# Performance work log

Hardware: AMD Instinct MI355X
Metric: run time of the kernel (lower is better)

## Reference

```python
import jax, jax.numpy as jnp
import numpy as np

N, E = 30000, 480000
D_IN, D_HID = 128, 256
NODE_CLS, EDGE_CLS, POLAR = 5, 2, 6
EPS = 1e-5

def layer_norm(x, g, b):
    mu = jnp.mean(x, axis=-1, keepdims=True)
    var = jnp.mean((x - mu) ** 2, axis=-1, keepdims=True)
    return g * (x - mu) / jnp.sqrt(var + EPS) + b

def sage_pool(h, src, dst, Wp, bp, Ws, bs, Wn, n_nodes):
    # DGL SAGEConv aggregator_type='pool': m = relu(fc_pool(h_src)); max over in-edges
    m = jax.nn.relu(h @ Wp + bp)              # [N, d_in]
    agg = jax.ops.segment_max(m[src], dst, num_segments=n_nodes)  # [N, d_in], -inf if no in-edges
    deg = jax.ops.segment_sum(jnp.ones((src.shape[0],), jnp.float32), dst, num_segments=n_nodes)
    h_neigh = jnp.where(deg[:, None] > 0, agg, 0.0)
    out = h @ Ws + bs + h_neigh @ Wn          # fc_self + fc_neigh
    return jax.nn.relu(out)                   # activation=F.relu

def setup_inputs() -> dict:
    key = jax.random.key(0)
    ks = jax.random.split(key, 24)
    p = lambda k, shape, fan: jax.random.normal(k, shape, jnp.float32) / np.sqrt(fan)
    return {
        "h": jax.random.normal(ks[0], (N, D_IN), jnp.float32),
        "efeat": jax.random.normal(ks[1], (E, POLAR), jnp.float32),
        "src": jax.random.randint(ks[2], (E,), 0, N, jnp.int32),
        "dst": jax.random.randint(ks[3], (E,), 0, N, jnp.int32),
        # encoder SAGEConv(128->256)
        "enc_Wpool": p(ks[4], (D_IN, D_IN), D_IN), "enc_bpool": jnp.zeros((D_IN,), jnp.float32),
        "enc_Wself": p(ks[5], (D_IN, D_HID), D_IN), "enc_bself": jnp.zeros((D_HID,), jnp.float32),
        "enc_Wneigh": p(ks[6], (D_IN, D_HID), D_IN),
        # node_pred: Linear(256,5) + LayerNorm(5)
        "np_W": p(ks[7], (D_HID, NODE_CLS), D_HID), "np_b": jnp.zeros((NODE_CLS,), jnp.float32),
        "np_g": jnp.ones((NODE_CLS,), jnp.float32), "np_beta": jnp.zeros((NODE_CLS,), jnp.float32),
        # edge predictor: Linear(528,256) + LN(256) + Linear(256,2)
        "ep_W1": p(ks[8], (2 * D_HID + 2 * NODE_CLS + POLAR, D_HID), 2 * D_HID + 16),
        "ep_b1": jnp.zeros((D_HID,), jnp.float32),
        "ep_g": jnp.ones((D_HID,), jnp.float32), "ep_beta": jnp.zeros((D_HID,), jnp.float32),
        "ep_W2": p(ks[9], (D_HID, EDGE_CLS), D_HID), "ep_b2": jnp.zeros((EDGE_CLS,), jnp.float32),
        # decoder SAGEConv(256->128)
        "dec_Wpool": p(ks[10], (D_HID, D_HID), D_HID), "dec_bpool": jnp.zeros((D_HID,), jnp.float32),
        "dec_Wself": p(ks[11], (D_HID, D_IN), D_HID), "dec_bself": jnp.zeros((D_IN,), jnp.float32),
        "dec_Wneigh": p(ks[12], (D_HID, D_IN), D_HID),
    }

def reference(h, efeat, src, dst,
              enc_Wpool, enc_bpool, enc_Wself, enc_bself, enc_Wneigh,
              np_W, np_b, np_g, np_beta,
              ep_W1, ep_b1, ep_g, ep_beta, ep_W2, ep_b2,
              dec_Wpool, dec_bpool, dec_Wself, dec_bself, dec_Wneigh):
    # encoder (drop_rate == 0 path)
    h1 = sage_pool(h, src, dst, enc_Wpool, enc_bpool, enc_Wself, enc_bself, enc_Wneigh, N)
    # node head
    node_pred = layer_norm(h1 @ np_W + np_b, np_g, np_beta)  # [N, 5]
    # edge head: gather-concat-MLP per edge
    cls_sm = jax.nn.softmax(node_pred, axis=1)               # softmax once, gather per edge
    x = jnp.concatenate([h1[src], cls_sm[src], efeat, h1[dst], cls_sm[dst]], axis=1)  # [E, 528]
    x = jax.nn.relu(layer_norm(x @ ep_W1 + ep_b1, ep_g, ep_beta))
    edges_pred = x @ ep_W2 + ep_b2                           # dropout is identity in eval
    # decoder (uses original graph, input h1)
    h2 = sage_pool(h1, src, dst, dec_Wpool, dec_bpool, dec_Wself, dec_bself, dec_Wneigh, N)
    return (node_pred, edges_pred, h2)
```

## Files before the change

### kernel.cpp

```cpp
#include <hip/hip_runtime.h>

typedef unsigned short u16;
typedef unsigned int u32;
typedef __bf16 bf16_t;
typedef bf16_t bf16x8 __attribute__((ext_vector_type(8)));
typedef float f32x4 __attribute__((ext_vector_type(4)));
typedef float f32x2 __attribute__((ext_vector_type(2)));

#define N_NODES 30000
#define N_EDGES 480000

static __device__ __forceinline__ float b2f(u16 u) {
  return __uint_as_float(((u32)u) << 16);
}
static __device__ __forceinline__ float b2f_lo(u32 w) {
  return __uint_as_float(w << 16);
}
static __device__ __forceinline__ float b2f_hi(u32 w) {
  return __uint_as_float(w & 0xffff0000u);
}
static __device__ __forceinline__ u16 f2b(float f) {
  u32 x = __float_as_uint(f);
  u32 r = (x + 0x7fffu + ((x >> 16) & 1u)) >> 16;
  return (u16)r;
}

__global__ __launch_bounds__(256) void init_sniff_deg(const u16* __restrict__ h,
                                                      int* __restrict__ flag,
                                                      int* __restrict__ deg) {
  int i = blockIdx.x * 256 + threadIdx.x;
  if (i < N_NODES) deg[i] = 0;
  if (blockIdx.x == 0) {
    int t = threadIdx.x;
    int bad = 0;
#pragma unroll
    for (int j = 0; j < 4; j++) {
      u32 e = ((u32)h[t * 4 + j] >> 7) & 0xFFu;
      if (e >= 0x8Eu) bad = 1;
    }
    int r = __syncthreads_or(bad);
    if (t == 0) *flag = r ? 1 : 0;
  }
}

struct ConvDesc { const void* s; u16* d; int n; int off; };
struct ConvTab { ConvDesc e[20]; int total; };

__global__ __launch_bounds__(256) void conv_all(
    const int* __restrict__ dstE, int* __restrict__ deg,
    const void* __restrict__ hsrc, u16* __restrict__ c_h,
    const void* __restrict__ efsrc, u16* __restrict__ c_ef,
    ConvTab tab, const int* __restrict__ flag) {
  int b = blockIdx.x;
  const int t = threadIdx.x;
  if (b < 1875) {
    int e = b * 256 + t;
    if (e < N_EDGES) atomicAdd(&deg[dstE[e]], 1);
    return;
  }
  b -= 1875;
  const int f = *flag;
  if (b < 3750) {
    int i = b * 256 + t;
    if (f) {
      float4 v = ((const float4*)hsrc)[i];
      uint2 o;
      o.x = (u32)f2b(v.x) | ((u32)f2b(v.y) << 16);
      o.y = (u32)f2b(v.z) | ((u32)f2b(v.w) << 16);
      ((uint2*)c_h)[i] = o;
    } else {
      ((uint2*)c_h)[i] = ((const uint2*)hsrc)[i];
    }
    return;
  }
  b -= 3750;
  if (b < 2813) {
    int i = b * 256 + t;
    if (i < 720000) {
      if (f) {
        float4 v = ((const float4*)efsrc)[i];
        uint2 o;
        o.x = (u32)f2b(v.x) | ((u32)f2b(v.y) << 16);
        o.y = (u32)f2b(v.z) | ((u32)f2b(v.w) << 16);
        ((uint2*)c_ef)[i] = o;
      } else {
        ((uint2*)c_ef)[i] = ((const uint2*)efsrc)[i];
      }
    }
    return;
  }
  b -= 2813;
  int i = b * 256 + t;
  if (i >= tab.total) return;
#pragma unroll 1
  for (int a = 0; a < 20; a++) {
    int j = i - tab.e[a].off;
    if (j >= 0 && j < tab.e[a].n) {
      if (f) tab.e[a].d[j] = f2b(((const float*)tab.e[a].s)[j]);
      else tab.e[a].d[j] = ((const u16*)tab.e[a].s)[j];
      return;
    }
  }
}

__global__ __launch_bounds__(1024) void scan_off(const int* __restrict__ deg,
                                                 int* __restrict__ off,
                                                 int* __restrict__ cursor, int n) {
  __shared__ int wsum[16];
  const int t = threadIdx.x, lane = t & 63, wv = t >> 6;
  const int CH = 30;
  int base = t * CH;
  int v[CH];
  int s = 0;
#pragma unroll
  for (int j = 0; j < CH; j++) {
    int idx = base + j;
    int d = (idx < n) ? deg[idx] : 0;
    v[j] = s;
    s += d;
  }
  int x = s;
#pragma unroll
  for (int d = 1; d < 64; d <<= 1) {
    int y = __shfl_up(x, d, 64);
    if (lane >= d) x += y;
  }
  if (lane == 63) wsum[wv] = x;
  __syncthreads();
  int wadd = 0;
  for (int w = 0; w < wv; w++) wadd += wsum[w];
  int pref = (x - s) + wadd;
  if (t == 0) off[0] = 0;
#pragma unroll
  for (int j = 0; j < CH; j++) {
    int idx = base + j;
    if (idx < n) {
      int excl = pref + v[j];
      int incl = pref + ((j + 1 < CH) ? v[j + 1] : s);
      cursor[idx] = excl;
      off[idx + 1] = incl;
    }
  }
}

__global__ __launch_bounds__(256) void fill_csr(const int* __restrict__ src,
                                                const int* __restrict__ dst,
                                                int* __restrict__ cursor,
                                                int* __restrict__ esrc, int nE) {
  int e = blockIdx.x * 256 + threadIdx.x;
  if (e >= nE) return;
  int p = atomicAdd(&cursor[dst[e]], 1);
  esrc[p] = src[e];
}

#define MRG(r)                                                    \
  do {                                                            \
    a0 = max(a0, (r).x & 0xffffu); a1 = max(a1, (r).x >> 16);     \
    a2 = max(a2, (r).y & 0xffffu); a3 = max(a3, (r).y >> 16);     \
    a4 = max(a4, (r).z & 0xffffu); a5 = max(a5, (r).z >> 16);     \
    a6 = max(a6, (r).w & 0xffffu); a7 = max(a7, (r).w >> 16);     \
  } while (0)

__global__ __launch_bounds__(256) void agg128(const u16* __restrict__ m,
                                              const int* __restrict__ esrc,
                                              const int* __restrict__ off,
                                              u16* __restrict__ out) {
  int wv = threadIdx.x >> 6, lane = threadIdx.x & 63;
  int qd = lane >> 4, l = lane & 15;
  int n = blockIdx.x * 16 + wv * 4 + qd;
  if (n >= N_NODES) return;
  int i = off[n], s1 = off[n + 1];
  u32 a0 = 0, a1 = 0, a2 = 0, a3 = 0, a4 = 0, a5 = 0, a6 = 0, a7 = 0;
  for (; i + 3 < s1; i += 4) {
    int e0 = esrc[i], e1 = esrc[i + 1], e2 = esrc[i + 2], e3 = esrc[i + 3];
    uint4 r0 = *(const uint4*)(m + (size_t)e0 * 128 + l * 8);
    uint4 r1 = *(const uint4*)(m + (size_t)e1 * 128 + l * 8);
    uint4 r2 = *(const uint4*)(m + (size_t)e2 * 128 + l * 8);
    uint4 r3 = *(const uint4*)(m + (size_t)e3 * 128 + l * 8);
    MRG(r0); MRG(r1); MRG(r2); MRG(r3);
  }
  for (; i < s1; i++) {
    uint4 r0 = *(const uint4*)(m + (size_t)esrc[i] * 128 + l * 8);
    MRG(r0);
  }
  uint4 w;
  w.x = a0 | (a1 << 16); w.y = a2 | (a3 << 16);
  w.z = a4 | (a5 << 16); w.w = a6 | (a7 << 16);
  *(uint4*)(out + (size_t)n * 128 + l * 8) = w;
}

__global__ __launch_bounds__(256) void agg256(const u16* __restrict__ m,
                                              const int* __restrict__ esrc,
                                              const int* __restrict__ off,
                                              u16* __restrict__ out) {
  int wv = threadIdx.x >> 6, lane = threadIdx.x & 63;
  int half = lane >> 5, l = lane & 31;
  int n = blockIdx.x * 8 + wv * 2 + half;
  if (n >= N_NODES) return;
  int i = off[n], s1 = off[n + 1];
  u32 a0 = 0, a1 = 0, a2 = 0, a3 = 0, a4 = 0, a5 = 0, a6 = 0, a7 = 0;
  for (; i + 3 < s1; i += 4) {
    int e0 = esrc[i], e1 = esrc[i + 1], e2 = esrc[i + 2], e3 = esrc[i + 3];
    uint4 r0 = *(const uint4*)(m + (size_t)e0 * 256 + l * 8);
    uint4 r1 = *(const uint4*)(m + (size_t)e1 * 256 + l * 8);
    uint4 r2 = *(const uint4*)(m + (size_t)e2 * 256 + l * 8);
    uint4 r3 = *(const uint4*)(m + (size_t)e3 * 256 + l * 8);
    MRG(r0); MRG(r1); MRG(r2); MRG(r3);
  }
  for (; i < s1; i++) {
    uint4 r0 = *(const uint4*)(m + (size_t)esrc[i] * 256 + l * 8);
    MRG(r0);
  }
  uint4 w;
  w.x = a0 | (a1 << 16); w.y = a2 | (a3 << 16);
  w.z = a4 | (a5 << 16); w.w = a6 | (a7 << 16);
  *(uint4*)(out + (size_t)n * 256 + l * 8) = w;
}
#undef MRG

__global__ __launch_bounds__(256) void prep_weights(
    const u16* __restrict__ encWp, const u16* __restrict__ encWs, const u16* __restrict__ encWn,
    const u16* __restrict__ decWp, const u16* __restrict__ decWs, const u16* __restrict__ decWn,
    const u16* __restrict__ epW1, const u16* __restrict__ epb1,
    u16* __restrict__ wt_encpool, u16* __restrict__ wt_enc,
    u16* __restrict__ wt_decpool, u16* __restrict__ wt_dec,
    u16* __restrict__ wt_UV, u16* __restrict__ b512, float* __restrict__ swsum) {
  int b = blockIdx.x;
  const int t = threadIdx.x;
  if (b < 64) {
    int idx = b * 256 + t; int k = idx >> 7, n = idx & 127;
    wt_encpool[n * 128 + k] = encWp[k * 128 + n]; return;
  }
  b -= 64;
  if (b < 128) {
    int idx = b * 256 + t; int k = idx >> 8, n = idx & 255;
    wt_enc[n * 256 + k] = encWs[k * 256 + n]; return;
  }
  b -= 128;
  if (b < 128) {
    int idx = b * 256 + t; int k = idx >> 8, n = idx & 255;
    wt_enc[n * 256 + 128 + k] = encWn[k * 256 + n]; return;
  }
  b -= 128;
  if (b < 256) {
    int idx = b * 256 + t; int k = idx >> 8, n = idx & 255;
    wt_decpool[n * 256 + k] = decWp[k * 256 + n]; return;
  }
  b -= 256;
  if (b < 128) {
    int idx = b * 256 + t; int k = idx >> 7, n = idx & 127;
    wt_dec[n * 512 + k] = decWs[k * 128 + n]; return;
  }
  b -= 128;
  if (b < 128) {
    int idx = b * 256 + t; int k = idx >> 7, n = idx & 127;
    wt_dec[n * 512 + 256 + k] = decWn[k * 128 + n]; return;
  }
  b -= 128;
  if (b < 512) {
    int n = b, n2 = n & 255, base = (n >= 256) ? 267 : 0;
    for (int kp = t; kp < 288; kp += 256) {
      u16 v = (kp < 261) ? epW1[(size_t)(base + kp) * 256 + n2] : (u16)0;
      wt_UV[(size_t)n * 288 + kp] = v;
    }
    return;
  }
  b -= 512;
  if (b < 2) {
    int i = b * 256 + t;
    b512[i] = (i < 256) ? epb1[i] : (u16)0; return;
  }
  int k = t >> 5, l32 = t & 31;
  if (k < 6) {
    uint4 v = *(const uint4*)(epW1 + (size_t)(261 + k) * 256 + l32 * 8);
    float s = b2f_lo(v.x) + b2f_hi(v.x) + b2f_lo(v.y) + b2f_hi(v.y) +
              b2f_lo(v.z) + b2f_hi(v.z) + b2f_lo(v.w) + b2f_hi(v.w);
#pragma unroll
    for (int m = 1; m < 32; m <<= 1) s += __shfl_xor(s, m, 64);
    if (l32 == 0) swsum[k] = s;
  }
}

__global__ __launch_bounds__(256) void gemm_mfma(
    const u16* __restrict__ A0, const u16* __restrict__ A1, int K0, int K1,
    const u16* __restrict__ Bt, const u16* __restrict__ bias, int do_relu,
    u16* __restrict__ C, float* __restrict__ Cf, const int* __restrict__ flag,
    int M, int Nld) {
  __shared__ __align__(16) u16 As[128 * 40];
  __shared__ __align__(16) u16 Bs[128 * 40];
  const int t = threadIdx.x;
  const int lane = t & 63, wv = t >> 6;
  const int wm = wv & 1, wn = wv >> 1;
  const int r = lane & 15, q = lane >> 4;
  const int bm = blockIdx.x, bn = blockIdx.y;
  const int Ktot = K0 + K1;
  const bool usef = (Cf != nullptr) && (*flag != 0);

  f32x4 acc[4][4];
#pragma unroll
  for (int i = 0; i < 4; i++)
#pragma unroll
    for (int j = 0; j < 4; j++) acc[i][j] = (f32x4){0.f, 0.f, 0.f, 0.f};

  for (int kc = 0; kc < Ktot; kc += 32) {
#pragma unroll
    for (int h = 0; h < 2; h++) {
      int idx = t + h * 256;
      int rr = idx >> 2, qq = idx & 3;
      int rowg = bm * 128 + rr;
      uint4 av = make_uint4(0, 0, 0, 0);
      if (rowg < M) {
        const u16* p = (kc < K0) ? (A0 + (size_t)rowg * K0 + kc)
                                 : (A1 + (size_t)rowg * K1 + (kc - K0));
        av = *(const uint4*)(p + qq * 8);
      }
      *(uint4*)&As[rr * 40 + qq * 8] = av;
      int ng = bn * 128 + rr;
      uint4 bv = *(const uint4*)(Bt + (size_t)ng * Ktot + kc + qq * 8);
      *(uint4*)&Bs[rr * 40 + qq * 8] = bv;
    }
    __syncthreads();
    bf16x8 af[4], bfm[4];
#pragma unroll
    for (int mi = 0; mi < 4; mi++)
      af[mi] = *(const bf16x8*)&As[(wm * 64 + mi * 16 + r) * 40 + q * 8];
#pragma unroll
    for (int ni = 0; ni < 4; ni++)
      bfm[ni] = *(const bf16x8*)&Bs[(wn * 64 + ni * 16 + r) * 40 + q * 8];
#pragma unroll
    for (int mi = 0; mi < 4; mi++)
#pragma unroll
      for (int ni = 0; ni < 4; ni++)
        acc[mi][ni] = __builtin_amdgcn_mfma_f32_16x16x32_bf16(af[mi], bfm[ni], acc[mi][ni], 0, 0, 0);
    __syncthreads();
  }

  float bv[4];
#pragma unroll
  for (int ni = 0; ni < 4; ni++)
    bv[ni] = bias ? b2f(bias[bn * 128 + wn * 64 + ni * 16 + r]) : 0.f;
#pragma unroll
  for (int mi = 0; mi < 4; mi++) {
#pragma unroll
    for (int i = 0; i < 4; i++) {
      int rowg = bm * 128 + wm * 64 + mi * 16 + q * 4 + i;
      if (rowg >= M) continue;
#pragma unroll
      for (int ni = 0; ni < 4; ni++) {
        int colg = bn * 128 + wn * 64 + ni * 16 + r;
        float v = acc[mi][ni][i] + bv[ni];
        if (do_relu) v = v > 0.f ? v : 0.f;
        if (usef) Cf[(size_t)rowg * Nld + colg] = v;
        else C[(size_t)rowg * Nld + colg] = f2b(v);
      }
    }
  }
}

__global__ __launch_bounds__(256) void node_head(
    const u16* __restrict__ h1, const u16* __restrict__ W, const u16* __restrict__ b,
    const u16* __restrict__ g, const u16* __restrict__ beta,
    u16* __restrict__ outN, float* __restrict__ outNf, const int* __restrict__ flag,
    u16* __restrict__ smOut) {
  __shared__ float Wl[256 * 5];
  __shared__ float bl[5], gl[5], betal[5];
  int t = threadIdx.x;
#pragma unroll
  for (int c = 0; c < 5; c++) Wl[t * 5 + c] = b2f(W[t * 5 + c]);
  if (t < 5) { bl[t] = b2f(b[t]); gl[t] = b2f(g[t]); betal[t] = b2f(beta[t]); }
  __syncthreads();
  int n = blockIdx.x * 256 + t;
  if (n >= N_NODES) return;
  const bool usef = (*flag != 0);
  float acc[5] = {0.f, 0.f, 0.f, 0.f, 0.f};
  const u16* hp = h1 + (size_t)n * 256;
  for (int k8 = 0; k8 < 32; k8++) {
    uint4 v = *(const uint4*)(hp + k8 * 8);
    u32 wds[4] = {v.x, v.y, v.z, v.w};
#pragma unroll
    for (int h = 0; h < 4; h++) {
      float x0 = b2f_lo(wds[h]), x1 = b2f_hi(wds[h]);
      int k = k8 * 8 + h * 2;
#pragma unroll
      for (int c = 0; c < 5; c++)
        acc[c] += x0 * Wl[k * 5 + c] + x1 * Wl[(k + 1) * 5 + c];
    }
  }
  float x[5], mu = 0.f;
#pragma unroll
  for (int c = 0; c < 5; c++) { x[c] = acc[c] + bl[c]; mu += x[c]; }
  mu *= 0.2f;
  float var = 0.f;
#pragma unroll
  for (int c = 0; c < 5; c++) { float d = x[c] - mu; var += d * d; }
  var *= 0.2f;
  float rstd = rsqrtf(fmaxf(var, 0.f) + 1e-5f);
  float v5[5], mx = -1e30f;
#pragma unroll
  for (int c = 0; c < 5; c++) {
    v5[c] = gl[c] * (x[c] - mu) * rstd + betal[c];
    if (usef) outNf[(size_t)n * 5 + c] = v5[c];
    else outN[(size_t)n * 5 + c] = f2b(v5[c]);
    mx = fmaxf(mx, v5[c]);
  }
  float s = 0.f, ex[5];
#pragma unroll
  for (int c = 0; c < 5; c++) { ex[c] = __expf(v5[c] - mx); s += ex[c]; }
  float inv = 1.f / s;
  u16 row[32];
#pragma unroll
  for (int c = 0; c < 5; c++) row[c] = f2b(ex[c] * inv);
#pragma unroll
  for (int c = 5; c < 32; c++) row[c] = 0;
#pragma unroll
  for (int c = 0; c < 4; c++)
    *(uint4*)(smOut + (size_t)n * 32 + c * 8) = *(const uint4*)&row[c * 8];
}

__global__ __launch_bounds__(256) void rowsum_uv(const u16* __restrict__ UV,
                                                 float2* __restrict__ Srow) {
  int wv = threadIdx.x >> 6, lane = threadIdx.x & 63;
  int n = blockIdx.x * 4 + wv;
  if (n >= N_NODES) return;
  uint4 v = *(const uint4*)(UV + (size_t)n * 512 + lane * 8);
  float s = b2f_lo(v.x) + b2f_hi(v.x) + b2f_lo(v.y) + b2f_hi(v.y) +
            b2f_lo(v.z) + b2f_hi(v.z) + b2f_lo(v.w) + b2f_hi(v.w);
#pragma unroll
  for (int m = 1; m < 32; m <<= 1) s += __shfl_xor(s, m, 64);
  if (lane == 0) Srow[n].x = s;
  if (lane == 32) Srow[n].y = s;
}

__global__ __launch_bounds__(256) void edge_mean(
    const int* __restrict__ src, const int* __restrict__ dst,
    const u16* __restrict__ ef, const float2* __restrict__ Srow,
    const float* __restrict__ swsum, uint4* __restrict__ recs) {
  int p = blockIdx.x * 256 + threadIdx.x;
  if (p >= 240000) {
    if (p < 240016) {
      uint4 z = make_uint4(0, 0, 0, 0);
      recs[(size_t)p * 3 + 0] = z;
      recs[(size_t)p * 3 + 1] = z;
      recs[(size_t)p * 3 + 2] = z;
    }
    return;
  }
  int e = p * 2;
  int s0 = src[e], s1 = src[e + 1];
  int d0 = dst[e], d1 = dst[e + 1];
  const u32* efp = (const u32*)(ef + (size_t)e * 6);
  u32 f0 = efp[0], f1 = efp[1], f2 = efp[2], f3 = efp[3], f4 = efp[4], f5 = efp[5];
  float xa[6] = {b2f_lo(f0), b2f_hi(f0), b2f_lo(f1), b2f_hi(f1), b2f_lo(f2), b2f_hi(f2)};
  float xb[6] = {b2f_lo(f3), b2f_hi(f3), b2f_lo(f4), b2f_hi(f4), b2f_lo(f5), b2f_hi(f5)};
  float sw[6];
#pragma unroll
  for (int k = 0; k < 6; k++) sw[k] = swsum[k];
  float m0 = Srow[s0].x + Srow[d0].y;
  float m1 = Srow[s1].x + Srow[d1].y;
#pragma unroll
  for (int k = 0; k < 6; k++) { m0 += xa[k] * sw[k]; m1 += xb[k] * sw[k]; }
  m0 *= (1.f / 256.f);
  m1 *= (1.f / 256.f);
  uint4 ra, rb, rc;
  ra.x = (u32)s0; ra.y = (u32)d0; ra.z = (u32)s1; ra.w = (u32)d1;
  rb.x = __float_as_uint(m0); rb.y = __float_as_uint(m1); rb.z = f0; rb.w = f1;
  rc.x = f2; rc.y = f3; rc.z = f4; rc.w = f5;
  recs[(size_t)p * 3 + 0] = ra;
  recs[(size_t)p * 3 + 1] = rb;
  recs[(size_t)p * 3 + 2] = rc;
}

__global__ __launch_bounds__(256) void edge_pt(
    const u16* __restrict__ UV, const uint4* __restrict__ recs,
    const u16* __restrict__ w1raw,
    const u16* __restrict__ g, const u16* __restrict__ beta,
    const u16* __restrict__ w2, const u16* __restrict__ b2,
    u16* __restrict__ outE, float* __restrict__ outEf, const int* __restrict__ flag) {
  const int t = threadIdx.x;
  const int lane = t & 63, wv = t >> 6;
  const int c0 = lane * 4;
  const int grp = (lane >> 4) & 3;
  f32x2 wefA[6], wefB[6];
#pragma unroll
  for (int k = 0; k < 6; k++) {
    u32 wa = *(const u32*)(w1raw + (size_t)(261 + k) * 256 + c0);
    u32 wb = *(const u32*)(w1raw + (size_t)(261 + k) * 256 + c0 + 2);
    wefA[k] = (f32x2){b2f_lo(wa), b2f_hi(wa)};
    wefB[k] = (f32x2){b2f_lo(wb), b2f_hi(wb)};
  }
  f32x2 glA = (f32x2){b2f(g[c0]), b2f(g[c0 + 1])};
  f32x2 glB = (f32x2){b2f(g[c0 + 2]), b2f(g[c0 + 3])};
  f32x2 blA = (f32x2){b2f(beta[c0]), b2f(beta[c0 + 1])};
  f32x2 blB = (f32x2){b2f(beta[c0 + 2]), b2f(beta[c0 + 3])};
  float w20[4], w21[4];
#pragma unroll
  for (int j = 0; j < 4; j++) {
    w20[j] = b2f(w2[(c0 + j) * 2]); w21[j] = b2f(w2[(c0 + j) * 2 + 1]);
  }
  const float b20 = b2f(b2[0]), b21 = b2f(b2[1]);
  const float bsel = (grp & 1) ? b21 : b20;
  const bool usef = (*flag != 0);
  const f32x2 zero2 = (f32x2){0.f, 0.f};

  const int pb = __builtin_amdgcn_readfirstlane((blockIdx.x * 4 + wv) * 16);
  const uint4* rp = recs + (size_t)pb * 3;
  uint4 r0a = rp[0], r0b = rp[1], r0c = rp[2];
  uint4 r1a = rp[3], r1b = rp[4], r1c = rp[5];
  uint2 gua = *(const uint2*)(UV + ((size_t)r0a.x << 9) + c0);
  uint2 gva = *(const uint2*)(UV + ((size_t)r0a.y << 9) + 256 + c0);
  uint2 gub = *(const uint2*)(UV + ((size_t)r0a.z << 9) + c0);
  uint2 gvb = *(const uint2*)(UV + ((size_t)r0a.w << 9) + 256 + c0);
#pragma unroll 2
  for (int it = 0; it < 16; ++it) {
    const int e = (pb + it) * 2;
    uint2 hua = *(const uint2*)(UV + ((size_t)r1a.x << 9) + c0);
    uint2 hva = *(const uint2*)(UV + ((size_t)r1a.y << 9) + 256 + c0);
    uint2 hub = *(const uint2*)(UV + ((size_t)r1a.z << 9) + c0);
    uint2 hvb = *(const uint2*)(UV + ((size_t)r1a.w << 9) + 256 + c0);
    uint4 r2a = rp[3 * it + 6], r2b = rp[3 * it + 7], r2c = rp[3 * it + 8];

    const float ma = __uint_as_float(r0b.x), mb = __uint_as_float(r0b.y);
    float xa[6] = {b2f_lo(r0b.z), b2f_hi(r0b.z), b2f_lo(r0b.w), b2f_hi(r0b.w),
                   b2f_lo(r0c.x), b2f_hi(r0c.x)};
    float xb[6] = {b2f_lo(r0c.y), b2f_hi(r0c.y), b2f_lo(r0c.z), b2f_hi(r0c.z),
                   b2f_lo(r0c.w), b2f_hi(r0c.w)};

    f32x2 yaA = (f32x2){b2f_lo(gua.x), b2f_hi(gua.x)} + (f32x2){b2f_lo(gva.x), b2f_hi(gva.x)};
    f32x2 yaB = (f32x2){b2f_lo(gua.y), b2f_hi(gua.y)} + (f32x2){b2f_lo(gva.y), b2f_hi(gva.y)};
    f32x2 ybA = (f32x2){b2f_lo(gub.x), b2f_hi(gub.x)} + (f32x2){b2f_lo(gvb.x), b2f_hi(gvb.x)};
    f32x2 ybB = (f32x2){b2f_lo(gub.y), b2f_hi(gub.y)} + (f32x2){b2f_lo(gvb.y), b2f_hi(gvb.y)};
#pragma unroll
    for (int k = 0; k < 6; k++) {
      yaA += xa[k] * wefA[k];
      yaB += xa[k] * wefB[k];
      ybA += xb[k] * wefA[k];
      ybB += xb[k] * wefB[k];
    }
    float pqa = yaA.x * yaA.x;
    pqa += yaA.y * yaA.y; pqa += yaB.x * yaB.x; pqa += yaB.y * yaB.y;
    float pqb = ybA.x * ybA.x;
    pqb += ybA.y * ybA.y; pqb += ybB.x * ybB.x; pqb += ybB.y * ybB.y;
    pqa += __shfl_xor(pqa, 32, 64);
    pqb += __shfl_xor(pqb, 32, 64);
    float z = (lane < 32) ? pqa : pqb;
#pragma unroll
    for (int m = 16; m >= 1; m >>= 1) z += __shfl_xor(z, m, 64);
    float zz = __shfl_xor(z, 32, 64);
    float pqa_t = (lane < 32) ? z : zz;
    float pqb_t = (lane < 32) ? zz : z;
    float rsa = rsqrtf(fmaxf(pqa_t * (1.f / 256.f) - ma * ma, 0.f) + 1e-5f);
    float rsb = rsqrtf(fmaxf(pqb_t * (1.f / 256.f) - mb * mb, 0.f) + 1e-5f);
    f32x2 nAa = __builtin_elementwise_max((yaA - ma) * rsa * glA + blA, zero2);
    f32x2 nAb = __builtin_elementwise_max((yaB - ma) * rsa * glB + blB, zero2);
    f32x2 nBa = __builtin_elementwise_max((ybA - mb) * rsb * glA + blA, zero2);
    f32x2 nBb = __builtin_elementwise_max((ybB - mb) * rsb * glB + blB, zero2);
    float p0a = nAa.x * w20[0], p1a = nAa.x * w21[0];
    p0a += nAa.y * w20[1]; p1a += nAa.y * w21[1];
    p0a += nAb.x * w20[2]; p1a += nAb.x * w21[2];
    p0a += nAb.y * w20[3]; p1a += nAb.y * w21[3];
    float p0b = nBa.x * w20[0], p1b = nBa.x * w21[0];
    p0b += nBa.y * w20[1]; p1b += nBa.y * w21[1];
    p0b += nBb.x * w20[2]; p1b += nBb.x * w21[2];
    p0b += nBb.y * w20[3]; p1b += nBb.y * w21[3];
    p0a += __shfl_xor(p0a, 32, 64); p1a += __shfl_xor(p1a, 32, 64);
    p0b += __shfl_xor(p0b, 32, 64); p1b += __shfl_xor(p1b, 32, 64);
    p0a += __shfl_xor(p0a, 16, 64); p1a += __shfl_xor(p1a, 16, 64);
    p0b += __shfl_xor(p0b, 16, 64); p1b += __shfl_xor(p1b, 16, 64);
    float w = (grp & 2) ? ((grp & 1) ? p1b : p0b) : ((grp & 1) ? p1a : p0a);
#pragma unroll
    for (int m = 8; m >= 1; m >>= 1) w += __shfl_xor(w, m, 64);
    if ((lane & 15) == 0) {
      float val = w + bsel;
      size_t oi = (size_t)e * 2 + grp;
      if (usef) outEf[oi] = val;
      else outE[oi] = f2b(val);
    }
    r0a = r1a; r0b = r1b; r0c = r1c;
    r1a = r2a; r1b = r2b; r1c = r2c;
    gua = hua; gva = hva; gub = hub; gvb = hvb;
  }
}

extern "C" void kernel_launch(void* const* d_in, const int* in_sizes, int n_in,
                              void* d_out, int out_size, void* d_ws, size_t ws_size,
                              hipStream_t stream) {
  char* wp = (char*)d_ws;
  auto alloc = [&](size_t bytes) -> char* {
    char* p = wp; wp += (bytes + 255) & ~(size_t)255; return p;
  };
  int* flag       = (int*)alloc(256);
  u16* c_h        = (u16*)alloc((size_t)N_NODES * 128 * 2);
  u16* c_ef       = (u16*)alloc((size_t)N_EDGES * 6 * 2);
  static const int pidx[20] = {4,5,6,7,8, 9,10,11,12, 13,14,15,16,17,18, 19,20,21,22,23};
  static const int pn[20]   = {16384,128,32768,256,32768, 1280,5,5,5,
                               135168,256,256,256,512,2, 65536,256,32768,128,32768};
  u16* cp[20];
  for (int a = 0; a < 20; a++) cp[a] = (u16*)alloc((size_t)pn[a] * 2);

  u16* wt_encpool = (u16*)alloc(128 * 128 * 2);
  u16* wt_enc     = (u16*)alloc(256 * 256 * 2);
  u16* wt_decpool = (u16*)alloc(256 * 256 * 2);
  u16* wt_dec     = (u16*)alloc(128 * 512 * 2);
  u16* wt_UV      = (u16*)alloc(512 * 288 * 2);
  u16* b512       = (u16*)alloc(512 * 2);
  float2* Srow    = (float2*)alloc((size_t)N_NODES * 8);
  float* swsum_b  = (float*)alloc(64);
  u16* m_buf      = (u16*)alloc((size_t)N_NODES * 256 * 2);
  u16* aggb       = (u16*)alloc((size_t)N_NODES * 256 * 2);
  u16* UVbuf      = m_buf;
  u16* h1b        = (u16*)alloc((size_t)N_NODES * 256 * 2);
  u16* smb32      = (u16*)alloc((size_t)N_NODES * 32 * 2);
  int* deg        = (int*)alloc((size_t)N_NODES * 4);
  int* off        = (int*)alloc((size_t)(N_NODES + 1) * 4);
  int* cursor     = (int*)alloc((size_t)N_NODES * 4);
  int* esrc       = (int*)alloc((size_t)N_EDGES * 4);
  uint4* recs     = (uint4*)alloc(((size_t)240000 * 3 + 64) * 16);

  const int* src = (const int*)d_in[2];
  const int* dst = (const int*)d_in[3];

  u16* outN = (u16*)d_out;
  u16* outE = outN + (size_t)N_NODES * 5;
  u16* outH = outN + 1110000;
  float* outNf = (float*)d_out;
  float* outEf = outNf + (size_t)N_NODES * 5;
  float* outHf = outNf + 1110000;

  init_sniff_deg<<<118, 256, 0, stream>>>((const u16*)d_in[0], flag, deg);
  ConvTab tab;
  int off_a = 0;
  for (int a = 0; a < 20; a++) {
    tab.e[a].s = d_in[pidx[a]]; tab.e[a].d = cp[a]; tab.e[a].n = pn[a]; tab.e[a].off = off_a;
    off_a += pn[a];
  }
  tab.total = off_a;
  int conv_blocks = 1875 + 3750 + 2813 + (off_a + 255) / 256;
  conv_all<<<conv_blocks, 256, 0, stream>>>(dst, deg, d_in[0], c_h, d_in[1], c_ef, tab, flag);

  const u16 *enc_Wpool = cp[0], *enc_bpool = cp[1], *enc_Wself = cp[2], *enc_bself = cp[3],
            *enc_Wneigh = cp[4], *np_W = cp[5], *np_b = cp[6], *np_g = cp[7], *np_beta = cp[8],
            *ep_W1 = cp[9], *ep_b1 = cp[10], *ep_g = cp[11], *ep_beta = cp[12],
            *ep_W2 = cp[13], *ep_b2 = cp[14], *dec_Wpool = cp[15], *dec_bpool = cp[16],
            *dec_Wself = cp[17], *dec_bself = cp[18], *dec_Wneigh = cp[19];

  scan_off<<<1, 1024, 0, stream>>>(deg, off, cursor, N_NODES);
  fill_csr<<<1875, 256, 0, stream>>>(src, dst, cursor, esrc, N_EDGES);

  prep_weights<<<1347, 256, 0, stream>>>(enc_Wpool, enc_Wself, enc_Wneigh,
                                         dec_Wpool, dec_Wself, dec_Wneigh,
                                         ep_W1, ep_b1,
                                         wt_encpool, wt_enc, wt_decpool, wt_dec,
                                         wt_UV, b512, swsum_b);

  gemm_mfma<<<dim3(235, 1), 256, 0, stream>>>(c_h, nullptr, 128, 0, wt_encpool,
                                              enc_bpool, 1, m_buf, nullptr, flag, N_NODES, 128);
  agg128<<<1875, 256, 0, stream>>>(m_buf, esrc, off, aggb);
  gemm_mfma<<<dim3(235, 2), 256, 0, stream>>>(c_h, aggb, 128, 128, wt_enc,
                                              enc_bself, 1, h1b, nullptr, flag, N_NODES, 256);
  node_head<<<118, 256, 0, stream>>>(h1b, np_W, np_b, np_g, np_beta, outN, outNf, flag, smb32);
  gemm_mfma<<<dim3(235, 4), 256, 0, stream>>>(h1b, smb32, 256, 32, wt_UV,
                                              b512, 0, UVbuf, nullptr, flag, N_NODES, 512);
  rowsum_uv<<<7500, 256, 0, stream>>>(UVbuf, Srow);
  edge_mean<<<938, 256, 0, stream>>>(src, dst, c_ef, Srow, swsum_b, recs);
  edge_pt<<<3750, 256, 0, stream>>>(UVbuf, recs, ep_W1, ep_g, ep_beta, ep_W2, ep_b2,
                                    outE, outEf, flag);
  gemm_mfma<<<dim3(235, 2), 256, 0, stream>>>(h1b, nullptr, 256, 0, wt_decpool,
                                              dec_bpool, 1, m_buf, nullptr, flag, N_NODES, 256);
  agg256<<<3750, 256, 0, stream>>>(m_buf, esrc, off, aggb);
  gemm_mfma<<<dim3(235, 1), 256, 0, stream>>>(h1b, aggb, 256, 256, wt_dec,
                                              dec_bself, 1, outH, outHf, flag, N_NODES, 128);
}
```

Before: 467.4 us.

## Column-slice max aggregation, merge CSR fill with weight prep, simplify edge prefetch

```diff
diff --git a/kernel.cpp b/kernel.cpp
--- a/kernel.cpp
+++ b/kernel.cpp
@@ -143,14 +143,88 @@
   }
 }
 
-__global__ __launch_bounds__(256) void fill_csr(const int* __restrict__ src,
-                                                const int* __restrict__ dst,
-                                                int* __restrict__ cursor,
-                                                int* __restrict__ esrc, int nE) {
-  int e = blockIdx.x * 256 + threadIdx.x;
-  if (e >= nE) return;
-  int p = atomicAdd(&cursor[dst[e]], 1);
-  esrc[p] = src[e];
+static __device__ void prep_body(
+    int b, int t,
+    const u16* __restrict__ encWp, const u16* __restrict__ encWs, const u16* __restrict__ encWn,
+    const u16* __restrict__ decWp, const u16* __restrict__ decWs, const u16* __restrict__ decWn,
+    const u16* __restrict__ epW1, const u16* __restrict__ epb1,
+    u16* __restrict__ wt_encpool, u16* __restrict__ wt_enc,
+    u16* __restrict__ wt_decpool, u16* __restrict__ wt_dec,
+    u16* __restrict__ wt_UV, u16* __restrict__ b512, float* __restrict__ swsum) {
+  if (b < 64) {
+    int idx = b * 256 + t; int k = idx >> 7, n = idx & 127;
+    wt_encpool[n * 128 + k] = encWp[k * 128 + n]; return;
+  }
+  b -= 64;
+  if (b < 128) {
+    int idx = b * 256 + t; int k = idx >> 8, n = idx & 255;
+    wt_enc[n * 256 + k] = encWs[k * 256 + n]; return;
+  }
+  b -= 128;
+  if (b < 128) {
+    int idx = b * 256 + t; int k = idx >> 8, n = idx & 255;
+    wt_enc[n * 256 + 128 + k] = encWn[k * 256 + n]; return;
+  }
+  b -= 128;
+  if (b < 256) {
+    int idx = b * 256 + t; int k = idx >> 8, n = idx & 255;
+    wt_decpool[n * 256 + k] = decWp[k * 256 + n]; return;
+  }
+  b -= 256;
+  if (b < 128) {
+    int idx = b * 256 + t; int k = idx >> 7, n = idx & 127;
+    wt_dec[n * 512 + k] = decWs[k * 128 + n]; return;
+  }
+  b -= 128;
+  if (b < 128) {
+    int idx = b * 256 + t; int k = idx >> 7, n = idx & 127;
+    wt_dec[n * 512 + 256 + k] = decWn[k * 128 + n]; return;
+  }
+  b -= 128;
+  if (b < 512) {
+    int n = b, n2 = n & 255, base = (n >= 256) ? 267 : 0;
+    for (int kp = t; kp < 288; kp += 256) {
+      u16 v = (kp < 261) ? epW1[(size_t)(base + kp) * 256 + n2] : (u16)0;
+      wt_UV[(size_t)n * 288 + kp] = v;
+    }
+    return;
+  }
+  b -= 512;
+  if (b < 2) {
+    int i = b * 256 + t;
+    b512[i] = (i < 256) ? epb1[i] : (u16)0; return;
+  }
+  int k = t >> 5, l32 = t & 31;
+  if (k < 6) {
+    uint4 v = *(const uint4*)(epW1 + (size_t)(261 + k) * 256 + l32 * 8);
+    float s = b2f_lo(v.x) + b2f_hi(v.x) + b2f_lo(v.y) + b2f_hi(v.y) +
+              b2f_lo(v.z) + b2f_hi(v.z) + b2f_lo(v.w) + b2f_hi(v.w);
+#pragma unroll
+    for (int m = 1; m < 32; m <<= 1) s += __shfl_xor(s, m, 64);
+    if (l32 == 0) swsum[k] = s;
+  }
+}
+
+__global__ __launch_bounds__(256) void fill_prep(
+    const int* __restrict__ src, const int* __restrict__ dst,
+    int* __restrict__ cursor, int* __restrict__ esrc,
+    const u16* __restrict__ encWp, const u16* __restrict__ encWs, const u16* __restrict__ encWn,
+    const u16* __restrict__ decWp, const u16* __restrict__ decWs, const u16* __restrict__ decWn,
+    const u16* __restrict__ epW1, const u16* __restrict__ epb1,
+    u16* __restrict__ wt_encpool, u16* __restrict__ wt_enc,
+    u16* __restrict__ wt_decpool, u16* __restrict__ wt_dec,
+    u16* __restrict__ wt_UV, u16* __restrict__ b512, float* __restrict__ swsum) {
+  int b = blockIdx.x;
+  if (b < 1875) {
+    int e = b * 256 + threadIdx.x;
+    if (e < N_EDGES) {
+      int p = atomicAdd(&cursor[dst[e]], 1);
+      esrc[p] = src[e];
+    }
+    return;
+  }
+  prep_body(b - 1875, threadIdx.x, encWp, encWs, encWn, decWp, decWs, decWn,
+            epW1, epb1, wt_encpool, wt_enc, wt_decpool, wt_dec, wt_UV, b512, swsum);
 }
 
 #define MRG(r)                                                    \
@@ -161,125 +235,68 @@
     a6 = max(a6, (r).w & 0xffffu); a7 = max(a7, (r).w >> 16);     \
   } while (0)
 
-__global__ __launch_bounds__(256) void agg128(const u16* __restrict__ m,
-                                              const int* __restrict__ esrc,
-                                              const int* __restrict__ off,
-                                              u16* __restrict__ out) {
-  int wv = threadIdx.x >> 6, lane = threadIdx.x & 63;
-  int qd = lane >> 4, l = lane & 15;
-  int n = blockIdx.x * 16 + wv * 4 + qd;
+__global__ __launch_bounds__(256) void agg128cs(const u16* __restrict__ m,
+                                                const int* __restrict__ esrc,
+                                                const int* __restrict__ off,
+                                                u16* __restrict__ out) {
+  int b = blockIdx.x;
+  int sl = b & 3, grp = b >> 2;
+  int t = threadIdx.x;
+  int n = grp * 64 + (t >> 2);
   if (n >= N_NODES) return;
+  int colb = sl * 32 + (t & 3) * 8;
+  const u16* mb = m + colb;
   int i = off[n], s1 = off[n + 1];
   u32 a0 = 0, a1 = 0, a2 = 0, a3 = 0, a4 = 0, a5 = 0, a6 = 0, a7 = 0;
   for (; i + 3 < s1; i += 4) {
     int e0 = esrc[i], e1 = esrc[i + 1], e2 = esrc[i + 2], e3 = esrc[i + 3];
-    uint4 r0 = *(const uint4*)(m + (size_t)e0 * 128 + l * 8);
-    uint4 r1 = *(const uint4*)(m + (size_t)e1 * 128 + l * 8);
-    uint4 r2 = *(const uint4*)(m + (size_t)e2 * 128 + l * 8);
-    uint4 r3 = *(const uint4*)(m + (size_t)e3 * 128 + l * 8);
+    uint4 r0 = *(const uint4*)(mb + (size_t)e0 * 128);
+    uint4 r1 = *(const uint4*)(mb + (size_t)e1 * 128);
+    uint4 r2 = *(const uint4*)(mb + (size_t)e2 * 128);
+    uint4 r3 = *(const uint4*)(mb + (size_t)e3 * 128);
     MRG(r0); MRG(r1); MRG(r2); MRG(r3);
   }
   for (; i < s1; i++) {
-    uint4 r0 = *(const uint4*)(m + (size_t)esrc[i] * 128 + l * 8);
+    uint4 r0 = *(const uint4*)(mb + (size_t)esrc[i] * 128);
     MRG(r0);
   }
   uint4 w;
   w.x = a0 | (a1 << 16); w.y = a2 | (a3 << 16);
   w.z = a4 | (a5 << 16); w.w = a6 | (a7 << 16);
-  *(uint4*)(out + (size_t)n * 128 + l * 8) = w;
-}
-
-__global__ __launch_bounds__(256) void agg256(const u16* __restrict__ m,
-                                              const int* __restrict__ esrc,
-                                              const int* __restrict__ off,
-                                              u16* __restrict__ out) {
-  int wv = threadIdx.x >> 6, lane = threadIdx.x & 63;
-  int half = lane >> 5, l = lane & 31;
-  int n = blockIdx.x * 8 + wv * 2 + half;
+  *(uint4*)(out + (size_t)n * 128 + colb) = w;
+}
+
+__global__ __launch_bounds__(256) void agg256cs(const u16* __restrict__ m,
+                                                const int* __restrict__ esrc,
+                                                const int* __restrict__ off,
+                                                u16* __restrict__ out) {
+  int b = blockIdx.x;
+  int sl = b & 7, grp = b >> 3;
+  int t = threadIdx.x;
+  int n = grp * 64 + (t >> 2);
   if (n >= N_NODES) return;
+  int colb = sl * 32 + (t & 3) * 8;
+  const u16* mb = m + colb;
   int i = off[n], s1 = off[n + 1];
   u32 a0 = 0, a1 = 0, a2 = 0, a3 = 0, a4 = 0, a5 = 0, a6 = 0, a7 = 0;
   for (; i + 3 < s1; i += 4) {
     int e0 = esrc[i], e1 = esrc[i + 1], e2 = esrc[i + 2], e3 = esrc[i + 3];
-    uint4 r0 = *(const uint4*)(m + (size_t)e0 * 256 + l * 8);
-    uint4 r1 = *(const uint4*)(m + (size_t)e1 * 256 + l * 8);
-    uint4 r2 = *(const uint4*)(m + (size_t)e2 * 256 + l * 8);
-    uint4 r3 = *(const uint4*)(m + (size_t)e3 * 256 + l * 8);
+    uint4 r0 = *(const uint4*)(mb + (size_t)e0 * 256);
+    uint4 r1 = *(const uint4*)(mb + (size_t)e1 * 256);
+    uint4 r2 = *(const uint4*)(mb + (size_t)e2 * 256);
+    uint4 r3 = *(const uint4*)(mb + (size_t)e3 * 256);
     MRG(r0); MRG(r1); MRG(r2); MRG(r3);
   }
   for (; i < s1; i++) {
-    uint4 r0 = *(const uint4*)(m + (size_t)esrc[i] * 256 + l * 8);
+    uint4 r0 = *(const uint4*)(mb + (size_t)esrc[i] * 256);
     MRG(r0);
   }
   uint4 w;
   w.x = a0 | (a1 << 16); w.y = a2 | (a3 << 16);
   w.z = a4 | (a5 << 16); w.w = a6 | (a7 << 16);
-  *(uint4*)(out + (size_t)n * 256 + l * 8) = w;
+  *(uint4*)(out + (size_t)n * 256 + colb) = w;
 }
 #undef MRG
-
-__global__ __launch_bounds__(256) void prep_weights(
-    const u16* __restrict__ encWp, const u16* __restrict__ encWs, const u16* __restrict__ encWn,
-    const u16* __restrict__ decWp, const u16* __restrict__ decWs, const u16* __restrict__ decWn,
-    const u16* __restrict__ epW1, const u16* __restrict__ epb1,
-    u16* __restrict__ wt_encpool, u16* __restrict__ wt_enc,
-    u16* __restrict__ wt_decpool, u16* __restrict__ wt_dec,
-    u16* __restrict__ wt_UV, u16* __restrict__ b512, float* __restrict__ swsum) {
-  int b = blockIdx.x;
-  const int t = threadIdx.x;
-  if (b < 64) {
-    int idx = b * 256 + t; int k = idx >> 7, n = idx & 127;
-    wt_encpool[n * 128 + k] = encWp[k * 128 + n]; return;
-  }
-  b -= 64;
-  if (b < 128) {
-    int idx = b * 256 + t; int k = idx >> 8, n = idx & 255;
-    wt_enc[n * 256 + k] = encWs[k * 256 + n]; return;
-  }
-  b -= 128;
-  if (b < 128) {
-    int idx = b * 256 + t; int k = idx >> 8, n = idx & 255;
-    wt_enc[n * 256 + 128 + k] = encWn[k * 256 + n]; return;
-  }
-  b -= 128;
-  if (b < 256) {
-    int idx = b * 256 + t; int k = idx >> 8, n = idx & 255;
-    wt_decpool[n * 256 + k] = decWp[k * 256 + n]; return;
-  }
-  b -= 256;
-  if (b < 128) {
-    int idx = b * 256 + t; int k = idx >> 7, n = idx & 127;
-    wt_dec[n * 512 + k] = decWs[k * 128 + n]; return;
-  }
-  b -= 128;
-  if (b < 128) {
-    int idx = b * 256 + t; int k = idx >> 7, n = idx & 127;
-    wt_dec[n * 512 + 256 + k] = decWn[k * 128 + n]; return;
-  }
-  b -= 128;
-  if (b < 512) {
-    int n = b, n2 = n & 255, base = (n >= 256) ? 267 : 0;
-    for (int kp = t; kp < 288; kp += 256) {
-      u16 v = (kp < 261) ? epW1[(size_t)(base + kp) * 256 + n2] : (u16)0;
-      wt_UV[(size_t)n * 288 + kp] = v;
-    }
-    return;
-  }
-  b -= 512;
-  if (b < 2) {
-    int i = b * 256 + t;
-    b512[i] = (i < 256) ? epb1[i] : (u16)0; return;
-  }
-  int k = t >> 5, l32 = t & 31;
-  if (k < 6) {
-    uint4 v = *(const uint4*)(epW1 + (size_t)(261 + k) * 256 + l32 * 8);
-    float s = b2f_lo(v.x) + b2f_hi(v.x) + b2f_lo(v.y) + b2f_hi(v.y) +
-              b2f_lo(v.z) + b2f_hi(v.z) + b2f_lo(v.w) + b2f_hi(v.w);
-#pragma unroll
-    for (int m = 1; m < 32; m <<= 1) s += __shfl_xor(s, m, 64);
-    if (l32 == 0) swsum[k] = s;
-  }
-}
 
 __global__ __launch_bounds__(256) void gemm_mfma(
     const u16* __restrict__ A0, const u16* __restrict__ A1, int K0, int K1,
@@ -504,31 +521,27 @@
 
   const int pb = __builtin_amdgcn_readfirstlane((blockIdx.x * 4 + wv) * 16);
   const uint4* rp = recs + (size_t)pb * 3;
-  uint4 r0a = rp[0], r0b = rp[1], r0c = rp[2];
-  uint4 r1a = rp[3], r1b = rp[4], r1c = rp[5];
-  uint2 gua = *(const uint2*)(UV + ((size_t)r0a.x << 9) + c0);
-  uint2 gva = *(const uint2*)(UV + ((size_t)r0a.y << 9) + 256 + c0);
-  uint2 gub = *(const uint2*)(UV + ((size_t)r0a.z << 9) + c0);
-  uint2 gvb = *(const uint2*)(UV + ((size_t)r0a.w << 9) + 256 + c0);
-#pragma unroll 2
+  uint4 ra = rp[0], rb = rp[1], rc = rp[2];
+#pragma unroll 1
   for (int it = 0; it < 16; ++it) {
     const int e = (pb + it) * 2;
-    uint2 hua = *(const uint2*)(UV + ((size_t)r1a.x << 9) + c0);
-    uint2 hva = *(const uint2*)(UV + ((size_t)r1a.y << 9) + 256 + c0);
-    uint2 hub = *(const uint2*)(UV + ((size_t)r1a.z << 9) + c0);
-    uint2 hvb = *(const uint2*)(UV + ((size_t)r1a.w << 9) + 256 + c0);
-    uint4 r2a = rp[3 * it + 6], r2b = rp[3 * it + 7], r2c = rp[3 * it + 8];
-
-    const float ma = __uint_as_float(r0b.x), mb = __uint_as_float(r0b.y);
-    float xa[6] = {b2f_lo(r0b.z), b2f_hi(r0b.z), b2f_lo(r0b.w), b2f_hi(r0b.w),
-                   b2f_lo(r0c.x), b2f_hi(r0c.x)};
-    float xb[6] = {b2f_lo(r0c.y), b2f_hi(r0c.y), b2f_lo(r0c.z), b2f_hi(r0c.z),
-                   b2f_lo(r0c.w), b2f_hi(r0c.w)};
-
-    f32x2 yaA = (f32x2){b2f_lo(gua.x), b2f_hi(gua.x)} + (f32x2){b2f_lo(gva.x), b2f_hi(gva.x)};
-    f32x2 yaB = (f32x2){b2f_lo(gua.y), b2f_hi(gua.y)} + (f32x2){b2f_lo(gva.y), b2f_hi(gva.y)};
-    f32x2 ybA = (f32x2){b2f_lo(gub.x), b2f_hi(gub.x)} + (f32x2){b2f_lo(gvb.x), b2f_hi(gvb.x)};
-    f32x2 ybB = (f32x2){b2f_lo(gub.y), b2f_hi(gub.y)} + (f32x2){b2f_lo(gvb.y), b2f_hi(gvb.y)};
+    uint4 ca = ra, cb = rb, cc = rc;
+    ra = rp[3 * it + 3]; rb = rp[3 * it + 4]; rc = rp[3 * it + 5];
+    const int s0 = (int)ca.x, d0 = (int)ca.y, s1 = (int)ca.z, d1 = (int)ca.w;
+    const float ma = __uint_as_float(cb.x), mb = __uint_as_float(cb.y);
+    float xa[6] = {b2f_lo(cb.z), b2f_hi(cb.z), b2f_lo(cb.w), b2f_hi(cb.w),
+                   b2f_lo(cc.x), b2f_hi(cc.x)};
+    float xb[6] = {b2f_lo(cc.y), b2f_hi(cc.y), b2f_lo(cc.z), b2f_hi(cc.z),
+                   b2f_lo(cc.w), b2f_hi(cc.w)};
+    uint2 ua = *(const uint2*)(UV + ((size_t)(u32)s0 << 9) + c0);
+    uint2 va = *(const uint2*)(UV + ((size_t)(u32)d0 << 9) + 256 + c0);
+    uint2 ub = *(const uint2*)(UV + ((size_t)(u32)s1 << 9) + c0);
+    uint2 vb = *(const uint2*)(UV + ((size_t)(u32)d1 << 9) + 256 + c0);
+
+    f32x2 yaA = (f32x2){b2f_lo(ua.x), b2f_hi(ua.x)} + (f32x2){b2f_lo(va.x), b2f_hi(va.x)};
+    f32x2 yaB = (f32x2){b2f_lo(ua.y), b2f_hi(ua.y)} + (f32x2){b2f_lo(va.y), b2f_hi(va.y)};
+    f32x2 ybA = (f32x2){b2f_lo(ub.x), b2f_hi(ub.x)} + (f32x2){b2f_lo(vb.x), b2f_hi(vb.x)};
+    f32x2 ybB = (f32x2){b2f_lo(ub.y), b2f_hi(ub.y)} + (f32x2){b2f_lo(vb.y), b2f_hi(vb.y)};
 #pragma unroll
     for (int k = 0; k < 6; k++) {
       yaA += xa[k] * wefA[k];
@@ -575,9 +588,6 @@
       if (usef) outEf[oi] = val;
       else outE[oi] = f2b(val);
     }
-    r0a = r1a; r0b = r1b; r0c = r1c;
-    r1a = r2a; r1b = r2b; r1c = r2c;
-    gua = hua; gva = hva; gub = hub; gvb = hvb;
   }
 }
 
@@ -644,17 +654,16 @@
             *dec_Wself = cp[17], *dec_bself = cp[18], *dec_Wneigh = cp[19];
 
   scan_off<<<1, 1024, 0, stream>>>(deg, off, cursor, N_NODES);
-  fill_csr<<<1875, 256, 0, stream>>>(src, dst, cursor, esrc, N_EDGES);
-
-  prep_weights<<<1347, 256, 0, stream>>>(enc_Wpool, enc_Wself, enc_Wneigh,
-                                         dec_Wpool, dec_Wself, dec_Wneigh,
-                                         ep_W1, ep_b1,
-                                         wt_encpool, wt_enc, wt_decpool, wt_dec,
-                                         wt_UV, b512, swsum_b);
+  fill_prep<<<1875 + 1347, 256, 0, stream>>>(src, dst, cursor, esrc,
+                                             enc_Wpool, enc_Wself, enc_Wneigh,
+                                             dec_Wpool, dec_Wself, dec_Wneigh,
+                                             ep_W1, ep_b1,
+                                             wt_encpool, wt_enc, wt_decpool, wt_dec,
+                                             wt_UV, b512, swsum_b);
 
   gemm_mfma<<<dim3(235, 1), 256, 0, stream>>>(c_h, nullptr, 128, 0, wt_encpool,
                                               enc_bpool, 1, m_buf, nullptr, flag, N_NODES, 128);
-  agg128<<<1875, 256, 0, stream>>>(m_buf, esrc, off, aggb);
+  agg128cs<<<469 * 4, 256, 0, stream>>>(m_buf, esrc, off, aggb);
   gemm_mfma<<<dim3(235, 2), 256, 0, stream>>>(c_h, aggb, 128, 128, wt_enc,
                                               enc_bself, 1, h1b, nullptr, flag, N_NODES, 256);
   node_head<<<118, 256, 0, stream>>>(h1b, np_W, np_b, np_g, np_beta, outN, outNf, flag, smb32);
@@ -666,7 +675,7 @@
                                     outE, outEf, flag);
   gemm_mfma<<<dim3(235, 2), 256, 0, stream>>>(h1b, nullptr, 256, 0, wt_decpool,
                                               dec_bpool, 1, m_buf, nullptr, flag, N_NODES, 256);
-  agg256<<<3750, 256, 0, stream>>>(m_buf, esrc, off, aggb);
+  agg256cs<<<469 * 8, 256, 0, stream>>>(m_buf, esrc, off, aggb);
   gemm_mfma<<<dim3(235, 1), 256, 0, stream>>>(h1b, aggb, 256, 256, wt_dec,
                                               dec_bself, 1, outH, outHf, flag, N_NODES, 128);
 }
```

Result: no change. 473.2 us (+1.2%).
